# Kernel tuning notes

Measured on AMD Instinct MI355X. Metric: run time of the kernel, lower is better.

Reference implementation:

```python
import jax, jax.numpy as jnp
import numpy as np

N = 100000   # nodes / embedding vocab
E = 1600000  # edges
D = 128      # feature dim
R = 7        # num relations
B = 4096     # matches
EPS = 1e-5


def setup_inputs() -> dict:
    key = jax.random.key(0)
    ks = jax.random.split(key, 12)
    s = 0.05
    return {
        "x": jnp.arange(N, dtype=jnp.int32),
        "edge_index": jax.random.randint(ks[0], (2, E), 0, N, dtype=jnp.int32),
        "edge_type": jax.random.randint(ks[1], (E,), 0, R, dtype=jnp.int32),
        "home": jax.random.randint(ks[2], (B,), 0, N, dtype=jnp.int32),
        "away": jax.random.randint(ks[3], (B,), 0, N, dtype=jnp.int32),
        "embed": jax.random.normal(ks[4], (N, D), jnp.float32) * s,
        "rel_w": jax.random.normal(ks[5], (3, R, D, D), jnp.float32) * s,
        "root_w": jax.random.normal(ks[6], (3, D, D), jnp.float32) * s,
        "conv_b": jnp.zeros((3, D), jnp.float32),
        "bn_gamma": jnp.ones((2, D), jnp.float32),
        "bn_beta": jnp.zeros((2, D), jnp.float32),
        "bn_mean": jnp.zeros((2, D), jnp.float32),
        "bn_var": jnp.ones((2, D), jnp.float32),
        "fc0_w": jax.random.normal(ks[7], (256, 2 * D), jnp.float32) * s,
        "fc0_b": jnp.zeros((256,), jnp.float32),
        "fc1_w": jax.random.normal(ks[8], (128, 256), jnp.float32) * s,
        "fc1_b": jnp.zeros((128,), jnp.float32),
        "fc2_w": jax.random.normal(ks[9], (3, 128), jnp.float32) * s,
        "fc2_b": jnp.zeros((3,), jnp.float32),
    }


def rgcn_conv(h, rel_w, root_w, bias, src, dst, seg):
    # PyG RGCNConv with aggr='mean': per-relation mean of source features,
    # aggregate-then-transform (valid since the relation transform is linear).
    n = h.shape[0]
    agg = jax.ops.segment_sum(h[src], seg, num_segments=n * R)      # [N*R, Din]
    cnt = jax.ops.segment_sum(jnp.ones((src.shape[0],), h.dtype), seg,
                              num_segments=n * R)                   # [N*R]
    agg = (agg / jnp.maximum(cnt, 1.0)[:, None]).reshape(n, R, -1)  # [N, R, Din]
    return jnp.einsum('nri,rio->no', agg, rel_w) + h @ root_w + bias


def reference(x, edge_index, edge_type, home, away, embed, rel_w, root_w, conv_b,
              bn_gamma, bn_beta, bn_mean, bn_var,
              fc0_w, fc0_b, fc1_w, fc1_b, fc2_w, fc2_b):
    src, dst = edge_index[0], edge_index[1]
    seg = dst.astype(jnp.int32) * R + edge_type  # combined (node, relation) id

    h = embed[x]  # [N, D]
    for l in range(2):
        h = rgcn_conv(h, rel_w[l], root_w[l], conv_b[l], src, dst, seg)
        h = (h - bn_mean[l]) * jax.lax.rsqrt(bn_var[l] + EPS) * bn_gamma[l] + bn_beta[l]
        h = jax.nn.relu(h)
    h = rgcn_conv(h, rel_w[2], root_w[2], conv_b[2], src, dst, seg)

    g = jnp.concatenate([h[home], h[away]], axis=1)  # [B, 2D]
    g = jax.nn.relu(g @ fc0_w.T + fc0_b)
    g = jax.nn.relu(g @ fc1_w.T + fc1_b)
    g = g @ fc2_w.T + fc2_b
    return jax.nn.log_softmax(g, axis=1)
```

## Files before the change

kernel.cpp:

```cpp
#include <hip/hip_runtime.h>
#include <hip/hip_bf16.h>

#define RR 7
#define EPSBN 1e-5f

typedef __attribute__((ext_vector_type(8))) __bf16 bf16x8;
typedef __attribute__((ext_vector_type(4))) float f32x4;
typedef __attribute__((ext_vector_type(2))) float f32x2;

__device__ __forceinline__ float uhi2f(unsigned int u) {
    union { unsigned int i; float f; } c; c.i = u; return c.f;
}
__device__ __forceinline__ unsigned short f2b(float f) {
    union { float f; unsigned int i; } c; c.f = f;
    unsigned int x = c.i;
    return (unsigned short)((x + 0x7fffu + ((x >> 16) & 1u)) >> 16);
}

__global__ void hist_k(const int* __restrict__ dst, const int* __restrict__ et,
                       int* __restrict__ cnt, int ne) {
    int e = blockIdx.x * 256 + threadIdx.x;
    if (e < ne) atomicAdd(&cnt[dst[e] * RR + et[e]], 1);
}
__global__ void scan1_k(const int* __restrict__ cnt, int* __restrict__ bsum, int n) {
    __shared__ int sh[256];
    int base = blockIdx.x << 10;
    int s = 0;
    for (int i = threadIdx.x; i < 1024; i += 256) { int idx = base + i; if (idx < n) s += cnt[idx]; }
    sh[threadIdx.x] = s; __syncthreads();
    for (int off = 128; off > 0; off >>= 1) {
        if (threadIdx.x < off) sh[threadIdx.x] += sh[threadIdx.x + off];
        __syncthreads();
    }
    if (threadIdx.x == 0) bsum[blockIdx.x] = sh[0];
}
__global__ void scan2_k(int* __restrict__ bsum, int nb) {
    __shared__ int sh[256];
    int t = threadIdx.x;
    int v[4]; int loc = 0;
#pragma unroll
    for (int i = 0; i < 4; ++i) { int idx = t * 4 + i; v[i] = (idx < nb) ? bsum[idx] : 0; loc += v[i]; }
    sh[t] = loc; __syncthreads();
    for (int off = 1; off < 256; off <<= 1) {
        int x = (t >= off) ? sh[t - off] : 0;
        __syncthreads();
        sh[t] += x;
        __syncthreads();
    }
    int ex = (t > 0) ? sh[t - 1] : 0;
#pragma unroll
    for (int i = 0; i < 4; ++i) { int idx = t * 4 + i; if (idx < nb) { int vv = v[i]; bsum[idx] = ex; ex += vv; } }
}
__global__ void scan3_k(const int* __restrict__ cnt, const int* __restrict__ boff,
                        int* __restrict__ ptr, int* __restrict__ cursor, int n, int total) {
    __shared__ int sh[256];
    int t = threadIdx.x;
    int base = (blockIdx.x << 10) + (t << 2);
    int v[4]; int loc = 0;
#pragma unroll
    for (int i = 0; i < 4; ++i) { int idx = base + i; v[i] = (idx < n) ? cnt[idx] : 0; loc += v[i]; }
    sh[t] = loc; __syncthreads();
    for (int off = 1; off < 256; off <<= 1) {
        int x = (t >= off) ? sh[t - off] : 0;
        __syncthreads();
        sh[t] += x;
        __syncthreads();
    }
    int ex = boff[blockIdx.x] + ((t > 0) ? sh[t - 1] : 0);
#pragma unroll
    for (int i = 0; i < 4; ++i) {
        int idx = base + i;
        if (idx < n) { ptr[idx] = ex; cursor[idx] = ex; ex += v[i]; }
    }
    if (blockIdx.x == 0 && t == 0) ptr[n] = total;
}
__global__ void scatter_k(const int* __restrict__ src, const int* __restrict__ dst,
                          const int* __restrict__ et, int* __restrict__ cursor,
                          int* __restrict__ ssorted, int ne) {
    int e = blockIdx.x * 256 + threadIdx.x;
    if (e < ne) {
        int seg = dst[e] * RR + et[e];
        int pos = atomicAdd(&cursor[seg], 1);
        ssorted[pos] = src[e];
    }
}

__global__ __launch_bounds__(256) void prep_w_k(const float* __restrict__ rel_w,
                                                const float* __restrict__ root_w,
                                                unsigned short* __restrict__ wall) {
    __shared__ unsigned short T[128][130];
    int l = blockIdx.x >> 3, kb = blockIdx.x & 7;
    const float* src = (kb < RR) ? rel_w + ((size_t)(l * RR + kb) << 14)
                                 : root_w + ((size_t)l << 14);
    int t = threadIdx.x;
    for (int c = t; c < 4096; c += 256) {
        float4 f = *(const float4*)(src + (c << 2));
        int i = c >> 5, o = (c & 31) << 2;
        T[i][o] = f2b(f.x); T[i][o+1] = f2b(f.y); T[i][o+2] = f2b(f.z); T[i][o+3] = f2b(f.w);
    }
    __syncthreads();
    unsigned short* dst = wall + ((size_t)blockIdx.x << 14);
    for (int c = t; c < 2048; c += 256) {
        int frag = c >> 6;
        int lane = c & 63;
        int ks = frag >> 3, nt = frag & 7;
        int o = (nt << 4) + (lane & 15);
        int ib = (ks << 5) + ((lane >> 4) << 3);
        uint4 o4;
        o4.x = (unsigned)T[ib+0][o] | ((unsigned)T[ib+1][o] << 16);
        o4.y = (unsigned)T[ib+2][o] | ((unsigned)T[ib+3][o] << 16);
        o4.z = (unsigned)T[ib+4][o] | ((unsigned)T[ib+5][o] << 16);
        o4.w = (unsigned)T[ib+6][o] | ((unsigned)T[ib+7][o] << 16);
        *(uint4*)(dst + (c << 3)) = o4;
    }
}
__global__ void prep_h_k(const int* __restrict__ x, const float* __restrict__ embed,
                         unsigned short* __restrict__ h, int n) {
    int i = blockIdx.x * 256 + threadIdx.x;
    if (i >= n * 16) return;
    int node = i >> 4, c8 = (i & 15) << 3;
    const float* e = embed + ((size_t)x[node] << 7) + c8;
    float4 f0 = *(const float4*)e;
    float4 f1 = *(const float4*)(e + 4);
    uint4 o4;
    o4.x = (unsigned)f2b(f0.x) | ((unsigned)f2b(f0.y) << 16);
    o4.y = (unsigned)f2b(f0.z) | ((unsigned)f2b(f0.w) << 16);
    o4.z = (unsigned)f2b(f1.x) | ((unsigned)f2b(f1.y) << 16);
    o4.w = (unsigned)f2b(f1.z) | ((unsigned)f2b(f1.w) << 16);
    *(uint4*)(h + ((size_t)node << 7) + c8) = o4;
}
__global__ void prep_bn_k(const float* __restrict__ conv_b,
                          const float* __restrict__ bn_g, const float* __restrict__ bn_b,
                          const float* __restrict__ bn_m, const float* __restrict__ bn_v,
                          float* __restrict__ AB) {
    int t = blockIdx.x * 128 + threadIdx.x;
    if (t >= 384) return;
    int l = t >> 7, j = t & 127;
    float A = 1.f, Bv = conv_b[(l << 7) + j];
    if (l < 2) {
        float sc = bn_g[(l << 7) + j] * rsqrtf(bn_v[(l << 7) + j] + EPSBN);
        A = sc;
        Bv = Bv * sc + (bn_b[(l << 7) + j] - bn_m[(l << 7) + j] * sc);
    }
    AB[(l << 8) + j] = A;
    AB[(l << 8) + 128 + j] = Bv;
}

#define PAIRF(w) ((f32x2){uhi2f((w) << 16), uhi2f((w) & 0xffff0000u)})
#define ACCP(b, u) { av2[(b)+0] += PAIRF((u).x); av2[(b)+1] += PAIRF((u).y); \
                     av2[(b)+2] += PAIRF((u).z); av2[(b)+3] += PAIRF((u).w); }

__global__ __launch_bounds__(256, 4) void layer_k(
    const unsigned short* __restrict__ h_in,
    unsigned short* __restrict__ h_out,
    const unsigned short* __restrict__ wfrag,
    const float* __restrict__ AB,
    const int* __restrict__ seg_ptr, const int* __restrict__ src_sorted,
    const int* __restrict__ list_a, const int* __restrict__ list_b, int listB,
    int nout, int bnrelu)
{
    const int tid  = threadIdx.x;
    const int wave = tid >> 6;
    const int lane = tid & 63;
    const int n16  = lane & 15;
    const int quad = lane >> 4;
    const int row0 = blockIdx.x << 6;
    const int gidx = row0 + (wave << 4) + n16;
    const bool valid = gidx < nout;
    int gnode = 0;
    if (valid) {
        gnode = list_a ? (gidx < listB ? list_a[gidx] : list_b[gidx - listB]) : gidx;
    }
    const int segbase = gnode * RR;

    f32x4 acc[8];
#pragma unroll
    for (int i = 0; i < 8; ++i) acc[i] = (f32x4){0.f, 0.f, 0.f, 0.f};

    int ecur = valid ? seg_ptr[segbase] : 0;

    const unsigned short* wl = wfrag + (lane << 3);

    for (int kb = 0; kb < 8; ++kb) {
        f32x2 av2[16];
#pragma unroll
        for (int i = 0; i < 16; ++i) av2[i] = (f32x2){0.f, 0.f};
        float scale = 1.f;
        if (valid) {
            int e0, e1;
            if (kb < RR) {
                e0 = ecur;
                e1 = seg_ptr[segbase + kb + 1];
                ecur = e1;
                int c = e1 - e0;
                if (c > 0) scale = __builtin_amdgcn_rcpf((float)c);
            } else { e0 = 0; e1 = 1; }
            for (int e = e0; e < e1; ++e) {
                int s = (kb < RR) ? src_sorted[e] : gnode;
                const unsigned short* hp = h_in + ((size_t)s << 7) + (quad << 3);
                uint4 u0 = *(const uint4*)(hp);
                uint4 u1 = *(const uint4*)(hp + 32);
                uint4 u2 = *(const uint4*)(hp + 64);
                uint4 u3 = *(const uint4*)(hp + 96);
                ACCP(0, u0); ACCP(4, u1); ACCP(8, u2); ACCP(12, u3);
            }
        }
        uint4 au[4];
#pragma unroll
        for (int ks = 0; ks < 4; ++ks) {
            unsigned pw[4];
#pragma unroll
            for (int m = 0; m < 4; ++m) {
                f32x2 q = av2[(ks << 2) + m] * scale;
                __hip_bfloat162 b2 = __float22bfloat162_rn(make_float2(q.x, q.y));
                unsigned u; __builtin_memcpy(&u, &b2, 4);
                pw[m] = u;
            }
            au[ks].x = pw[0]; au[ks].y = pw[1]; au[ks].z = pw[2]; au[ks].w = pw[3];
        }
        const unsigned short* wk = wl + (kb << 14);
#pragma unroll
        for (int ks = 0; ks < 4; ++ks) {
            bf16x8 af;
            __builtin_memcpy(&af, &au[ks], 16);
#pragma unroll
            for (int nt = 0; nt < 8; ++nt) {
                bf16x8 bfr = *(const bf16x8*)(wk + (((ks << 3) + nt) << 9));
                acc[nt] = __builtin_amdgcn_mfma_f32_16x16x32_bf16(af, bfr, acc[nt], 0, 0, 0);
            }
        }
    }

#pragma unroll
    for (int nt = 0; nt < 8; ++nt) {
        int j = (nt << 4) + n16;
        float Aj = AB[j];
        float Bj = AB[128 + j];
#pragma unroll
        for (int r = 0; r < 4; ++r) {
            int orow = row0 + (wave << 4) + (quad << 2) + r;
            if (orow < nout) {
                float v = acc[nt][r] * Aj + Bj;
                if (bnrelu) v = fmaxf(v, 0.f);
                h_out[((size_t)orow << 7) + j] = f2b(v);
            }
        }
    }
}

__global__ __launch_bounds__(256) void mlp_k(
    const unsigned short* __restrict__ hC,
    const float* __restrict__ w0, const float* __restrict__ bb0,
    const float* __restrict__ w1, const float* __restrict__ bb1,
    const float* __restrict__ w2, const float* __restrict__ bb2,
    float* __restrict__ out, int Bn)
{
    __shared__ __attribute__((aligned(16))) float g0[16][256];
    __shared__ __attribute__((aligned(16))) float g1[16][256];
    __shared__ float lg[16][4];
    int t = threadIdx.x;
    {
        int row = t >> 4;
        int cseg = (t & 15) << 4;
        int gr = (blockIdx.x << 4) + row;
        int gc = (gr < Bn) ? gr : 0;
        const unsigned short* sp = (cseg < 128) ? (hC + ((size_t)gc << 7) + cseg)
                                                : (hC + ((size_t)(Bn + gc) << 7) + (cseg - 128));
#pragma unroll
        for (int c8 = 0; c8 < 2; ++c8) {
            uint4 v = *(const uint4*)(sp + (c8 << 3));
            int base = cseg + (c8 << 3);
            g0[row][base+0] = uhi2f(v.x << 16); g0[row][base+1] = uhi2f(v.x & 0xffff0000u);
            g0[row][base+2] = uhi2f(v.y << 16); g0[row][base+3] = uhi2f(v.y & 0xffff0000u);
            g0[row][base+4] = uhi2f(v.z << 16); g0[row][base+5] = uhi2f(v.z & 0xffff0000u);
            g0[row][base+6] = uhi2f(v.w << 16); g0[row][base+7] = uhi2f(v.w & 0xffff0000u);
        }
    }
    __syncthreads();
    {
        float acc[16];
#pragma unroll
        for (int r = 0; r < 16; ++r) acc[r] = 0.f;
        const float* wr = w0 + (t << 8);
        for (int i = 0; i < 256; i += 4) {
            float4 w = *(const float4*)(wr + i);
#pragma unroll
            for (int r = 0; r < 16; ++r) {
                float4 g = *(const float4*)&g0[r][i];
                acc[r] += w.x * g.x + w.y * g.y + w.z * g.z + w.w * g.w;
            }
        }
        float bb = bb0[t];
#pragma unroll
        for (int r = 0; r < 16; ++r) g1[r][t] = fmaxf(acc[r] + bb, 0.f);
    }
    __syncthreads();
    {
        int o = t & 127, rg = t >> 7;
        float acc[8];
#pragma unroll
        for (int r = 0; r < 8; ++r) acc[r] = 0.f;
        const float* wr = w1 + (o << 8);
        for (int i = 0; i < 256; i += 4) {
            float4 w = *(const float4*)(wr + i);
#pragma unroll
            for (int r = 0; r < 8; ++r) {
                float4 g = *(const float4*)&g1[(rg << 3) + r][i];
                acc[r] += w.x * g.x + w.y * g.y + w.z * g.z + w.w * g.w;
            }
        }
        float bb = bb1[o];
#pragma unroll
        for (int r = 0; r < 8; ++r) g0[(rg << 3) + r][o] = fmaxf(acc[r] + bb, 0.f);
    }
    __syncthreads();
    if (t < 48) {
        int row = t / 3, cls = t - row * 3;
        const float* wr = w2 + (cls << 7);
        float a = 0.f;
        for (int i = 0; i < 128; i += 4) {
            float4 w = *(const float4*)(wr + i);
            float4 g = *(const float4*)&g0[row][i];
            a += w.x * g.x + w.y * g.y + w.z * g.z + w.w * g.w;
        }
        lg[row][cls] = a + bb2[cls];
    }
    __syncthreads();
    if (t < 16) {
        int gr = (blockIdx.x << 4) + t;
        if (gr < Bn) {
            float l0 = lg[t][0], l1 = lg[t][1], l2 = lg[t][2];
            float m = fmaxf(l0, fmaxf(l1, l2));
            float lse = m + logf(expf(l0 - m) + expf(l1 - m) + expf(l2 - m));
            out[gr * 3 + 0] = l0 - lse;
            out[gr * 3 + 1] = l1 - lse;
            out[gr * 3 + 2] = l2 - lse;
        }
    }
}

extern "C" void kernel_launch(void* const* d_in, const int* in_sizes, int n_in,
                              void* d_out, int out_size, void* d_ws, size_t ws_size,
                              hipStream_t stream) {
    const int*   x      = (const int*)d_in[0];
    const int*   eidx   = (const int*)d_in[1];
    const int*   etype  = (const int*)d_in[2];
    const int*   home   = (const int*)d_in[3];
    const int*   away   = (const int*)d_in[4];
    const float* embed  = (const float*)d_in[5];
    const float* rel_w  = (const float*)d_in[6];
    const float* root_w = (const float*)d_in[7];
    const float* conv_b = (const float*)d_in[8];
    const float* bn_g   = (const float*)d_in[9];
    const float* bn_b   = (const float*)d_in[10];
    const float* bn_m   = (const float*)d_in[11];
    const float* bn_v   = (const float*)d_in[12];
    const float* fc0w   = (const float*)d_in[13];
    const float* fc0b   = (const float*)d_in[14];
    const float* fc1w   = (const float*)d_in[15];
    const float* fc1b   = (const float*)d_in[16];
    const float* fc2w   = (const float*)d_in[17];
    const float* fc2b   = (const float*)d_in[18];
    float* out = (float*)d_out;

    const int N_ = in_sizes[0];
    const int E_ = in_sizes[2];
    const int B_ = in_sizes[3];
    const int NS = N_ * RR;

    char* ws = (char*)d_ws;
    auto alloc = [&](size_t bytes) -> char* {
        char* p = ws;
        ws += (bytes + 255) & ~(size_t)255;
        return p;
    };
    int* ptr         = (int*)alloc((size_t)(NS + 1) * 4);
    int* cursor      = (int*)alloc((size_t)NS * 4);
    int* bsum        = (int*)alloc(4096);
    int* src_sorted  = (int*)alloc((size_t)E_ * 4);
    unsigned short* wall = (unsigned short*)alloc((size_t)3 * 8 * 16384 * 2);
    unsigned short* hA   = (unsigned short*)alloc((size_t)N_ * 128 * 2);
    unsigned short* hB   = (unsigned short*)alloc((size_t)N_ * 128 * 2);
    unsigned short* hC   = (unsigned short*)alloc((size_t)2 * B_ * 128 * 2);
    float* AB        = (float*)alloc(3 * 256 * 4);

    const int nb = (NS + 1023) / 1024;

    (void)hipMemsetAsync(cursor, 0, (size_t)NS * 4, stream);
    hist_k<<<(E_ + 255) / 256, 256, 0, stream>>>(eidx + E_, etype, cursor, E_);
    scan1_k<<<nb, 256, 0, stream>>>(cursor, bsum, NS);
    scan2_k<<<1, 256, 0, stream>>>(bsum, nb);
    scan3_k<<<nb, 256, 0, stream>>>(cursor, bsum, ptr, cursor, NS, E_);
    scatter_k<<<(E_ + 255) / 256, 256, 0, stream>>>(eidx, eidx + E_, etype, cursor, src_sorted, E_);

    prep_w_k<<<24, 256, 0, stream>>>(rel_w, root_w, wall);
    prep_h_k<<<(N_ * 16 + 255) / 256, 256, 0, stream>>>(x, embed, hA, N_);
    prep_bn_k<<<3, 128, 0, stream>>>(conv_b, bn_g, bn_b, bn_m, bn_v, AB);

    const int lgrid = (N_ + 63) / 64;
    layer_k<<<lgrid, 256, 0, stream>>>(hA, hB, wall + 0 * 8 * 16384, AB + 0,
                                       ptr, src_sorted, nullptr, nullptr, 0, N_, 1);
    layer_k<<<lgrid, 256, 0, stream>>>(hB, hA, wall + 1 * 8 * 16384, AB + 256,
                                       ptr, src_sorted, nullptr, nullptr, 0, N_, 1);
    const int n3 = 2 * B_;
    layer_k<<<(n3 + 63) / 64, 256, 0, stream>>>(hA, hC, wall + 2 * 8 * 16384, AB + 512,
                                                ptr, src_sorted, home, away, B_, n3, 0);

    mlp_k<<<(B_ + 15) / 16, 256, 0, stream>>>(hC, fc0w, fc0b, fc1w, fc1b,
                                              fc2w, fc2b, out, B_);
}
```

Before: 671.9 us.

## Prefetch segment pointers and next-relation source indices in layer kernel; transpose MLP weights

The layer kernel now loads all eight segment pointers up front and, in a fully unrolled relation loop, prefetches the first four source indices of the next relation segment while the current one is gathered and multiplied. This is meant to hide the dependent pointer-then-index-then-row load chain. Source index reads may run past the segment end, so the index buffer is padded by 16 entries. Separately, the fc0 and fc1 weights are transposed in a prep kernel so MLP threads read weights coalesced, at the cost of scalar LDS reads of activations.

```diff
diff --git a/kernel.cpp b/kernel.cpp
--- a/kernel.cpp
+++ b/kernel.cpp
@@ -129,26 +129,43 @@
     o4.w = (unsigned)f2b(f1.z) | ((unsigned)f2b(f1.w) << 16);
     *(uint4*)(h + ((size_t)node << 7) + c8) = o4;
 }
-__global__ void prep_bn_k(const float* __restrict__ conv_b,
-                          const float* __restrict__ bn_g, const float* __restrict__ bn_b,
-                          const float* __restrict__ bn_m, const float* __restrict__ bn_v,
-                          float* __restrict__ AB) {
-    int t = blockIdx.x * 128 + threadIdx.x;
-    if (t >= 384) return;
-    int l = t >> 7, j = t & 127;
-    float A = 1.f, Bv = conv_b[(l << 7) + j];
-    if (l < 2) {
-        float sc = bn_g[(l << 7) + j] * rsqrtf(bn_v[(l << 7) + j] + EPSBN);
-        A = sc;
-        Bv = Bv * sc + (bn_b[(l << 7) + j] - bn_m[(l << 7) + j] * sc);
-    }
-    AB[(l << 8) + j] = A;
-    AB[(l << 8) + 128 + j] = Bv;
+__global__ void prep_misc_k(const float* __restrict__ fc0w, const float* __restrict__ fc1w,
+                            float* __restrict__ w0t, float* __restrict__ w1t,
+                            const float* __restrict__ conv_b,
+                            const float* __restrict__ bn_g, const float* __restrict__ bn_b,
+                            const float* __restrict__ bn_m, const float* __restrict__ bn_v,
+                            float* __restrict__ AB) {
+    int b = blockIdx.x;
+    if (b < 256) {
+        int idx = (b << 8) + threadIdx.x;
+        int o = idx & 255, i = idx >> 8;
+        w0t[idx] = fc0w[o * 256 + i];
+    } else if (b < 384) {
+        int idx = ((b - 256) << 8) + threadIdx.x;
+        int o = idx & 127, i = idx >> 7;
+        w1t[idx] = fc1w[o * 256 + i];
+    } else {
+        for (int t = threadIdx.x; t < 384; t += 256) {
+            int l = t >> 7, j = t & 127;
+            float A = 1.f, Bv = conv_b[(l << 7) + j];
+            if (l < 2) {
+                float sc = bn_g[(l << 7) + j] * rsqrtf(bn_v[(l << 7) + j] + EPSBN);
+                A = sc;
+                Bv = Bv * sc + (bn_b[(l << 7) + j] - bn_m[(l << 7) + j] * sc);
+            }
+            AB[(l << 8) + j] = A;
+            AB[(l << 8) + 128 + j] = Bv;
+        }
+    }
 }
 
 #define PAIRF(w) ((f32x2){uhi2f((w) << 16), uhi2f((w) & 0xffff0000u)})
 #define ACCP(b, u) { av2[(b)+0] += PAIRF((u).x); av2[(b)+1] += PAIRF((u).y); \
                      av2[(b)+2] += PAIRF((u).z); av2[(b)+3] += PAIRF((u).w); }
+#define GATH(s) { const unsigned short* hp = h_in + ((size_t)(s) << 7) + (quad << 3); \
+                  uint4 u0 = *(const uint4*)(hp);       uint4 u1 = *(const uint4*)(hp + 32); \
+                  uint4 u2 = *(const uint4*)(hp + 64);  uint4 u3 = *(const uint4*)(hp + 96); \
+                  ACCP(0, u0); ACCP(4, u1); ACCP(8, u2); ACCP(12, u3); }
 
 __global__ __launch_bounds__(256, 4) void layer_k(
     const unsigned short* __restrict__ h_in,
@@ -171,39 +188,52 @@
     if (valid) {
         gnode = list_a ? (gidx < listB ? list_a[gidx] : list_b[gidx - listB]) : gidx;
     }
-    const int segbase = gnode * RR;
+
+    int p[8];
+    {
+        int b = valid ? gnode * RR : 0;
+#pragma unroll
+        for (int i = 0; i < 8; ++i) p[i] = seg_ptr[b + i];
+    }
 
     f32x4 acc[8];
 #pragma unroll
     for (int i = 0; i < 8; ++i) acc[i] = (f32x4){0.f, 0.f, 0.f, 0.f};
 
-    int ecur = valid ? seg_ptr[segbase] : 0;
+    int sv0, sv1, sv2, sv3;
+    { int e0 = p[0]; sv0 = src_sorted[e0]; sv1 = src_sorted[e0+1];
+      sv2 = src_sorted[e0+2]; sv3 = src_sorted[e0+3]; }
 
     const unsigned short* wl = wfrag + (lane << 3);
 
+#pragma unroll
     for (int kb = 0; kb < 8; ++kb) {
         f32x2 av2[16];
 #pragma unroll
         for (int i = 0; i < 16; ++i) av2[i] = (f32x2){0.f, 0.f};
         float scale = 1.f;
-        if (valid) {
-            int e0, e1;
-            if (kb < RR) {
-                e0 = ecur;
-                e1 = seg_ptr[segbase + kb + 1];
-                ecur = e1;
-                int c = e1 - e0;
-                if (c > 0) scale = __builtin_amdgcn_rcpf((float)c);
-            } else { e0 = 0; e1 = 1; }
-            for (int e = e0; e < e1; ++e) {
-                int s = (kb < RR) ? src_sorted[e] : gnode;
-                const unsigned short* hp = h_in + ((size_t)s << 7) + (quad << 3);
-                uint4 u0 = *(const uint4*)(hp);
-                uint4 u1 = *(const uint4*)(hp + 32);
-                uint4 u2 = *(const uint4*)(hp + 64);
-                uint4 u3 = *(const uint4*)(hp + 96);
-                ACCP(0, u0); ACCP(4, u1); ACCP(8, u2); ACCP(12, u3);
-            }
+        int nv0 = 0, nv1 = 0, nv2 = 0, nv3 = 0;
+        if (kb < RR) {
+            if (kb < RR - 1) {
+                int en = p[kb + 1];
+                nv0 = src_sorted[en]; nv1 = src_sorted[en+1];
+                nv2 = src_sorted[en+2]; nv3 = src_sorted[en+3];
+            }
+            if (valid) {
+                int e0 = p[kb], e1 = p[kb + 1];
+                int cnt = e1 - e0;
+                if (cnt > 0) scale = __builtin_amdgcn_rcpf((float)cnt);
+                if (cnt > 0) GATH(sv0);
+                if (cnt > 1) GATH(sv1);
+                if (cnt > 2) GATH(sv2);
+                if (cnt > 3) GATH(sv3);
+                for (int e = e0 + 4; e < e1; ++e) {
+                    int s = src_sorted[e];
+                    GATH(s);
+                }
+            }
+        } else {
+            if (valid) GATH(gnode);
         }
         uint4 au[4];
 #pragma unroll
@@ -229,6 +259,7 @@
                 acc[nt] = __builtin_amdgcn_mfma_f32_16x16x32_bf16(af, bfr, acc[nt], 0, 0, 0);
             }
         }
+        sv0 = nv0; sv1 = nv1; sv2 = nv2; sv3 = nv3;
     }
 
 #pragma unroll
@@ -250,8 +281,8 @@
 
 __global__ __launch_bounds__(256) void mlp_k(
     const unsigned short* __restrict__ hC,
-    const float* __restrict__ w0, const float* __restrict__ bb0,
-    const float* __restrict__ w1, const float* __restrict__ bb1,
+    const float* __restrict__ w0t, const float* __restrict__ bb0,
+    const float* __restrict__ w1t, const float* __restrict__ bb1,
     const float* __restrict__ w2, const float* __restrict__ bb2,
     float* __restrict__ out, int Bn)
 {
@@ -281,14 +312,11 @@
         float acc[16];
 #pragma unroll
         for (int r = 0; r < 16; ++r) acc[r] = 0.f;
-        const float* wr = w0 + (t << 8);
-        for (int i = 0; i < 256; i += 4) {
-            float4 w = *(const float4*)(wr + i);
-#pragma unroll
-            for (int r = 0; r < 16; ++r) {
-                float4 g = *(const float4*)&g0[r][i];
-                acc[r] += w.x * g.x + w.y * g.y + w.z * g.z + w.w * g.w;
-            }
+#pragma unroll 4
+        for (int i = 0; i < 256; ++i) {
+            float w = w0t[(i << 8) + t];
+#pragma unroll
+            for (int r = 0; r < 16; ++r) acc[r] += w * g0[r][i];
         }
         float bb = bb0[t];
 #pragma unroll
@@ -300,14 +328,11 @@
         float acc[8];
 #pragma unroll
         for (int r = 0; r < 8; ++r) acc[r] = 0.f;
-        const float* wr = w1 + (o << 8);
-        for (int i = 0; i < 256; i += 4) {
-            float4 w = *(const float4*)(wr + i);
-#pragma unroll
-            for (int r = 0; r < 8; ++r) {
-                float4 g = *(const float4*)&g1[(rg << 3) + r][i];
-                acc[r] += w.x * g.x + w.y * g.y + w.z * g.z + w.w * g.w;
-            }
+#pragma unroll 4
+        for (int i = 0; i < 256; ++i) {
+            float w = w1t[(i << 7) + o];
+#pragma unroll
+            for (int r = 0; r < 8; ++r) acc[r] += w * g1[(rg << 3) + r][i];
         }
         float bb = bb1[o];
 #pragma unroll
@@ -377,12 +402,14 @@
     int* ptr         = (int*)alloc((size_t)(NS + 1) * 4);
     int* cursor      = (int*)alloc((size_t)NS * 4);
     int* bsum        = (int*)alloc(4096);
-    int* src_sorted  = (int*)alloc((size_t)E_ * 4);
+    int* src_sorted  = (int*)alloc((size_t)(E_ + 16) * 4);
     unsigned short* wall = (unsigned short*)alloc((size_t)3 * 8 * 16384 * 2);
     unsigned short* hA   = (unsigned short*)alloc((size_t)N_ * 128 * 2);
     unsigned short* hB   = (unsigned short*)alloc((size_t)N_ * 128 * 2);
     unsigned short* hC   = (unsigned short*)alloc((size_t)2 * B_ * 128 * 2);
     float* AB        = (float*)alloc(3 * 256 * 4);
+    float* w0t       = (float*)alloc(65536 * 4);
+    float* w1t       = (float*)alloc(32768 * 4);
 
     const int nb = (NS + 1023) / 1024;
 
@@ -395,7 +422,8 @@
 
     prep_w_k<<<24, 256, 0, stream>>>(rel_w, root_w, wall);
     prep_h_k<<<(N_ * 16 + 255) / 256, 256, 0, stream>>>(x, embed, hA, N_);
-    prep_bn_k<<<3, 128, 0, stream>>>(conv_b, bn_g, bn_b, bn_m, bn_v, AB);
+    prep_misc_k<<<385, 256, 0, stream>>>(fc0w, fc1w, w0t, w1t,
+                                         conv_b, bn_g, bn_b, bn_m, bn_v, AB);
 
     const int lgrid = (N_ + 63) / 64;
     layer_k<<<lgrid, 256, 0, stream>>>(hA, hB, wall + 0 * 8 * 16384, AB + 0,
@@ -406,6 +434,6 @@
     layer_k<<<(n3 + 63) / 64, 256, 0, stream>>>(hA, hC, wall + 2 * 8 * 16384, AB + 512,
                                                 ptr, src_sorted, home, away, B_, n3, 0);
 
-    mlp_k<<<(B_ + 15) / 16, 256, 0, stream>>>(hC, fc0w, fc0b, fc1w, fc1b,
+    mlp_k<<<(B_ + 15) / 16, 256, 0, stream>>>(hC, w0t, fc0b, w1t, fc1b,
                                               fc2w, fc2b, out, B_);
 }
```

After: 682.0 us. Within noise of the previous version (+1.5%).
